# Kernel tuning notes

Measured on AMD Instinct MI355X. Metric: run time of the kernel, lower is better.

The kernel has to match this reference:

```python
import jax, jax.numpy as jnp
import numpy as np

WS = (8, 8)          # window_size
HEADS = 8
DH = 64              # dim_head
SHIFT = (4, 4)
SCALE = DH ** -0.5


def setup_inputs() -> dict:
    key = jax.random.key(0)
    ks = jax.random.split(key, 5)
    dim = 64
    inner = HEADS * DH  # 512
    b, h, w = 4, 192, 192
    x = jax.random.normal(ks[0], (b, h, w, dim), dtype=jnp.float32)
    Wq = jax.random.normal(ks[1], (dim, inner), dtype=jnp.float32) * (dim ** -0.5)
    Wkv = jax.random.normal(ks[2], (dim, 2 * inner), dtype=jnp.float32) * (dim ** -0.5)
    Wo = jax.random.normal(ks[3], (inner, dim), dtype=jnp.float32) * (inner ** -0.5)
    bo = jnp.zeros((dim,), dtype=jnp.float32)
    seq_l = WS[0] * WS[1]
    pos_emb = jax.random.normal(ks[4], (1, HEADS, seq_l, seq_l), dtype=jnp.float32)
    return {"x": x, "Wq": Wq, "Wkv": Wkv, "Wo": Wo, "bo": bo, "pos_emb": pos_emb}


def reference(x, Wq, Wkv, Wo, bo, pos_emb):
    b, h, w, c = x.shape
    L = WS[0] * WS[1]  # 64 tokens per window
    if SHIFT[0] > 0:
        x = jnp.roll(x, shift=(-SHIFT[0], -SHIFT[1]), axis=(1, 2))
    # NOTE: original uses a raw .view() here (row-major reshape), NOT an 8x8
    # window partition. Replicate exactly.
    nw = b * (h // WS[0]) * (w // WS[1])
    x_inp = x.reshape(nw, L, c)                      # [nw, 64, c]
    q = x_inp @ Wq                                   # [nw, 64, inner]
    kv = x_inp @ Wkv
    k, v = jnp.split(kv, 2, axis=-1)
    # original: raw view (nw, L, inner) -> (nw, heads, L, dh) (not a transpose)
    q = q.reshape(nw, HEADS, L, DH) * SCALE
    k = k.reshape(nw, HEADS, L, DH)
    v = v.reshape(nw, HEADS, L, DH)
    sim = jnp.einsum('bhid,bhjd->bhij', q, k) + pos_emb
    attn = jax.nn.softmax(sim, axis=-1)
    out = jnp.einsum('bhij,bhjd->bhid', attn, v)     # [nw, heads, 64, dh]
    # original: raw view back to (nw, L, inner)
    out = out.reshape(nw, L, HEADS * DH)
    out = out @ Wo + bo                              # [nw, 64, c]
    out = out.reshape(b, h, w, c)
    if SHIFT[0] > 0:
        out = jnp.roll(out, shift=(SHIFT[0], SHIFT[1]), axis=(1, 2))
    return out
```

## Files before the change

kernel.cpp:

```cpp
#include <hip/hip_runtime.h>
#include <hip/hip_bf16.h>
#include <stdint.h>

typedef __attribute__((ext_vector_type(8))) short bf16x8;
typedef __attribute__((ext_vector_type(4))) short s16x4;
typedef __attribute__((ext_vector_type(4))) float f32x4;

#define THREADS 256
constexpr int NWIN = 2304;

constexpr int WCATT_E = 0;
constexpr int WOT_E   = 98304;
constexpr int POS_E   = 131072;
constexpr size_t WS_NEED = 327680;

__device__ __forceinline__ short f2bf(float f) {
  __hip_bfloat16 h = __float2bfloat16(f);
  return __builtin_bit_cast(short, h);
}
__device__ __forceinline__ float bf2f(short s) {
  uint32_t u = ((uint32_t)(uint16_t)s) << 16;
  return __builtin_bit_cast(float, u);
}
__device__ __forceinline__ int swz(int row, int h) {
  return ((((row ^ (row >> 2) ^ (row >> 3)) & 7) ^ h) << 4);
}

__global__ void wmsa_prep(const float* __restrict__ Wq, const float* __restrict__ Wkv,
                          const float* __restrict__ Wo, const float* __restrict__ pos,
                          short* __restrict__ ws) {
  int idx = blockIdx.x * 256 + threadIdx.x;
  if (idx < 32768) {
    int n = idx & 511, k = idx >> 9;
    ws[WCATT_E + n * 64 + k] = f2bf(Wq[k * 512 + n] * 0.125f);
  } else if (idx < 98304) {
    int j = idx - 32768;
    int nkv = j & 1023, k = j >> 10;
    ws[WCATT_E + (512 + nkv) * 64 + k] = f2bf(Wkv[k * 1024 + nkv]);
  } else if (idx < 131072) {
    int j = idx - 98304;
    int n = j & 63, k = j >> 6;
    ws[WOT_E + n * 512 + k] = f2bf(Wo[k * 64 + n]);
  } else if (idx < 163840) {
    int j = idx - 131072;
    ws[POS_E + j] = f2bf(pos[j]);
  }
}

__global__ __launch_bounds__(512, 2)
void wmsa_mfma4(const float* __restrict__ x, const float* __restrict__ bo,
                const short* __restrict__ ws, float* __restrict__ out) {
  extern __shared__ __align__(16) char lds[];
  const int tid = threadIdx.x;
  const int wv = tid >> 6;
  const int l  = tid & 63;
  const int lr = l & 15;
  const int lg = l >> 4;

  const int bid = blockIdx.x;
  const int q   = bid >> 2;
  const int hp  = bid & 3;

  bf16x8 xa[4][2];
  #pragma unroll
  for (int win = 0; win < 4; ++win) {
    int w   = 4 * q + win;
    int bb  = w / 576;
    int rem = (w % 576) * 64;
    int hh  = rem / 192;
    int ww0 = rem % 192;
    int src_h = (hh + 4) % 192;
    const float* xp = x + (size_t)(bb * 192 + src_h) * 12288;
    int tok = 16 * hp + lr;
    int sw = ww0 + tok + 4; if (sw >= 192) sw -= 192;
    const float* xq = xp + sw * 64;
    #pragma unroll
    for (int ks = 0; ks < 2; ++ks) {
      float4 a = *(const float4*)(xq + ks * 32 + lg * 8);
      float4 b = *(const float4*)(xq + ks * 32 + lg * 8 + 4);
      bf16x8 v;
      v[0] = f2bf(a.x); v[1] = f2bf(a.y); v[2] = f2bf(a.z); v[3] = f2bf(a.w);
      v[4] = f2bf(b.x); v[5] = f2bf(b.y); v[6] = f2bf(b.z); v[7] = f2bf(b.w);
      xa[win][ks] = v;
    }
  }

  #pragma unroll
  for (int t = 0; t < 8; ++t) {
    int nt = wv + 8 * t;
    int nload = nt * 16 + lr;
    bf16x8 b0 = *(const bf16x8*)(ws + WCATT_E + nload * 64 + lg * 8);
    bf16x8 b1 = *(const bf16x8*)(ws + WCATT_E + nload * 64 + 32 + lg * 8);
    const bool isQ = (t < 4);
    int i  = (lr & 7) * 8 + ((nt >> 2) & 7);
    int h2 = lr >> 3;
    int d0 = (nt & 3) * 16 + lg * 4;
    int off = (isQ ? 0 : 16384) + h2 * 8192 + i * 128 + ((d0 * 2) ^ swz(i, h2));
    #pragma unroll
    for (int win = 0; win < 4; ++win) {
      f32x4 acc = {0.f, 0.f, 0.f, 0.f};
      acc = __builtin_amdgcn_mfma_f32_16x16x32_bf16(b0, xa[win][0], acc, 0, 0, 0);
      acc = __builtin_amdgcn_mfma_f32_16x16x32_bf16(b1, xa[win][1], acc, 0, 0, 0);
      s16x4 pk;
      #pragma unroll
      for (int r = 0; r < 4; ++r) pk[r] = f2bf(acc[r]);
      *(s16x4*)(lds + win * 32768 + off) = pk;
    }
  }

  const int bq = wv & 3, aq = wv >> 2;
  f32x4 vacc[4][4];
  #pragma unroll
  for (int u = 0; u < 4; ++u) {
    int ntile = (aq * 4 + u) * 4 + bq;
    int nload = (64 + ntile) * 16 + lr;
    bf16x8 b0 = *(const bf16x8*)(ws + WCATT_E + nload * 64 + lg * 8);
    bf16x8 b1 = *(const bf16x8*)(ws + WCATT_E + nload * 64 + 32 + lg * 8);
    #pragma unroll
    for (int win = 0; win < 4; ++win) {
      f32x4 acc = {0.f, 0.f, 0.f, 0.f};
      acc = __builtin_amdgcn_mfma_f32_16x16x32_bf16(xa[win][0], b0, acc, 0, 0, 0);
      acc = __builtin_amdgcn_mfma_f32_16x16x32_bf16(xa[win][1], b1, acc, 0, 0, 0);
      vacc[win][u] = acc;
    }
  }
  __syncthreads();

  const int hl = (wv >> 1) & 1;
  const int ih = wv & 1;
  const int hglob = 2 * hp + hl;
  const int wbase = aq;

  s16x4 posr[2][4];
  #pragma unroll
  for (int it = 0; it < 2; ++it) {
    int i = (ih * 2 + it) * 16 + lr;
    const short* pp = ws + POS_E + hglob * 4096 + i * 64;
    #pragma unroll
    for (int jt = 0; jt < 4; ++jt)
      posr[it][jt] = *(const s16x4*)(pp + jt * 16 + lg * 4);
  }

  #pragma unroll
  for (int c = 0; c < 2; ++c) {
    char* ldw = lds + (wbase + 2 * c) * 32768;
    f32x4 s[2][4];
    #pragma unroll
    for (int it = 0; it < 2; ++it)
      #pragma unroll
      for (int jt = 0; jt < 4; ++jt) s[it][jt] = (f32x4){0.f, 0.f, 0.f, 0.f};

    #pragma unroll
    for (int ks = 0; ks < 2; ++ks) {
      bf16x8 kb[4], qa[2];
      #pragma unroll
      for (int jt = 0; jt < 4; ++jt) {
        int j = jt * 16 + lr;
        kb[jt] = *(const bf16x8*)(ldw + 16384 + hl * 8192 + j * 128 + ((ks * 64 + lg * 16) ^ swz(j, hl)));
      }
      #pragma unroll
      for (int it = 0; it < 2; ++it) {
        int i = (ih * 2 + it) * 16 + lr;
        qa[it] = *(const bf16x8*)(ldw + hl * 8192 + i * 128 + ((ks * 64 + lg * 16) ^ swz(i, hl)));
      }
      __builtin_amdgcn_s_setprio(1);
      #pragma unroll
      for (int it = 0; it < 2; ++it)
        #pragma unroll
        for (int jt = 0; jt < 4; ++jt)
          s[it][jt] = __builtin_amdgcn_mfma_f32_16x16x32_bf16(kb[jt], qa[it], s[it][jt], 0, 0, 0);
      __builtin_amdgcn_s_setprio(0);
    }

    #pragma unroll
    for (int it = 0; it < 2; ++it) {
      int i = (ih * 2 + it) * 16 + lr;
      float sum = 0.f;
      #pragma unroll
      for (int jt = 0; jt < 4; ++jt)
        #pragma unroll
        for (int r = 0; r < 4; ++r) {
          float pv = __expf(s[it][jt][r] + bf2f(posr[it][jt][r]));
          s[it][jt][r] = pv;
          sum += pv;
        }
      sum += __shfl_xor(sum, 16);
      sum += __shfl_xor(sum, 32);
      float rinv = 1.f / sum;
      #pragma unroll
      for (int jt = 0; jt < 4; ++jt) {
        s16x4 pk;
        #pragma unroll
        for (int r = 0; r < 4; ++r) pk[r] = f2bf(s[it][jt][r] * rinv);
        *(s16x4*)(ldw + hl * 8192 + i * 128 + ((jt * 32 + lg * 8) ^ swz(i, hl))) = pk;
      }
    }
  }
  __syncthreads();

  {
    int d = bq * 16 + lr;
    #pragma unroll
    for (int win = 0; win < 4; ++win)
      #pragma unroll
      for (int r = 0; r < 4; ++r) {
        int tl = lg * 4 + r;
        int h2 = tl >> 3;
        int jb = (tl & 7) * 16 + aq * 8;
        s16x4 pk;
        #pragma unroll
        for (int u = 0; u < 4; ++u) pk[u] = f2bf(vacc[win][u][r]);
        *(s16x4*)(lds + win * 32768 + 16384 + h2 * 8192 + d * 128 + (jb ^ swz(d, h2))) = pk;
      }
  }
  __syncthreads();

  bf16x8 wofr[16];
  #pragma unroll
  for (int ks = 0; ks < 16; ++ks)
    wofr[ks] = *(const bf16x8*)(ws + WOT_E + (bq * 16 + lr) * 512 + ks * 32 + lg * 8);

  #pragma unroll
  for (int c = 0; c < 2; ++c) {
    char* ldw = lds + (wbase + 2 * c) * 32768;
    f32x4 o[2][4];
    #pragma unroll
    for (int it = 0; it < 2; ++it)
      #pragma unroll
      for (int dt = 0; dt < 4; ++dt) o[it][dt] = (f32x4){0.f, 0.f, 0.f, 0.f};
    #pragma unroll
    for (int ks = 0; ks < 2; ++ks) {
      bf16x8 vb[4], pa[2];
      #pragma unroll
      for (int dt = 0; dt < 4; ++dt) {
        int d = dt * 16 + lr;
        vb[dt] = *(const bf16x8*)(ldw + 16384 + hl * 8192 + d * 128 + ((ks * 64 + lg * 16) ^ swz(d, hl)));
      }
      #pragma unroll
      for (int it = 0; it < 2; ++it) {
        int i = (ih * 2 + it) * 16 + lr;
        pa[it] = *(const bf16x8*)(ldw + hl * 8192 + i * 128 + ((ks * 64 + lg * 16) ^ swz(i, hl)));
      }
      __builtin_amdgcn_s_setprio(1);
      #pragma unroll
      for (int it = 0; it < 2; ++it)
        #pragma unroll
        for (int dt = 0; dt < 4; ++dt)
          o[it][dt] = __builtin_amdgcn_mfma_f32_16x16x32_bf16(vb[dt], pa[it], o[it][dt], 0, 0, 0);
      __builtin_amdgcn_s_setprio(0);
    }
    #pragma unroll
    for (int it = 0; it < 2; ++it) {
      int i  = (ih * 2 + it) * 16 + lr;
      int lm = 8 * hl + (i >> 3);
      int rp = lm * 8 + (i & 7);
      #pragma unroll
      for (int dt = 0; dt < 4; ++dt) {
        s16x4 pk;
        #pragma unroll
        for (int r = 0; r < 4; ++r) pk[r] = f2bf(o[it][dt][r]);
        *(s16x4*)(ldw + rp * 128 + ((dt * 32 + lg * 8) ^ swz(rp, 0))) = pk;
      }
    }
  }
  __syncthreads();

  f32x4 oacc0 = {0.f, 0.f, 0.f, 0.f};
  f32x4 oacc1 = {0.f, 0.f, 0.f, 0.f};
  #pragma unroll
  for (int ks = 0; ks < 16; ++ks) {
    int rp = lr * 8 + (ks >> 1);
    int boff = rp * 128 + (((ks & 1) * 64 + lg * 16) ^ swz(rp, 0));
    bf16x8 bA = *(const bf16x8*)(lds + wbase * 32768 + boff);
    bf16x8 bB = *(const bf16x8*)(lds + (wbase + 2) * 32768 + boff);
    oacc0 = __builtin_amdgcn_mfma_f32_16x16x32_bf16(wofr[ks], bA, oacc0, 0, 0, 0);
    oacc1 = __builtin_amdgcn_mfma_f32_16x16x32_bf16(wofr[ks], bB, oacc1, 0, 0, 0);
  }
  {
    int c0 = bq * 16 + lg * 4;
    float4 bo4 = *(const float4*)(bo + c0);
    int tok = 16 * hp + lr;
    #pragma unroll
    for (int c = 0; c < 2; ++c) {
      int w   = 4 * q + wbase + 2 * c;
      int bb  = w / 576;
      int rem = (w % 576) * 64;
      int hh  = rem / 192;
      int ww0 = rem % 192;
      int src_h = (hh + 4) % 192;
      float* orow = out + (size_t)(bb * 192 + src_h) * 12288;
      int sw = ww0 + tok + 4; if (sw >= 192) sw -= 192;
      f32x4 oa = c ? oacc1 : oacc0;
      float4 ov;
      ov.x = oa[0] + bo4.x; ov.y = oa[1] + bo4.y;
      ov.z = oa[2] + bo4.z; ov.w = oa[3] + bo4.w;
      *(float4*)(orow + sw * 64 + c0) = ov;
    }
  }
}

__global__ __launch_bounds__(THREADS, 2)
void wmsa_mfma(const float* __restrict__ x, const float* __restrict__ bo,
               const short* __restrict__ ws, float* __restrict__ out) {
  __shared__ __align__(16) char lds[65536];
  const int tid = threadIdx.x;
  const int wv = tid >> 6;
  const int l  = tid & 63;
  const int lr = l & 15;
  const int lg = l >> 4;

  const int bid = blockIdx.x;
  const int p   = bid >> 2;
  const int hp  = bid & 3;

  const float* xrow[2];
  float* orow[2];
  int ww0a[2];
  #pragma unroll
  for (int win = 0; win < 2; ++win) {
    int w   = 2 * p + win;
    int t0  = w * 64;
    int bb  = t0 / 36864;
    int rem = t0 % 36864;
    int hh  = rem / 192;
    ww0a[win] = rem % 192;
    int src_h = (hh + 4) % 192;
    xrow[win] = x + (size_t)(bb * 192 + src_h) * 12288;
    orow[win] = out + (size_t)(bb * 192 + src_h) * 12288;
  }

  bf16x8 xa[2][2];
  #pragma unroll
  for (int win = 0; win < 2; ++win) {
    int tok = 16 * hp + lr;
    int sw = ww0a[win] + tok + 4; if (sw >= 192) sw -= 192;
    const float* xp = xrow[win] + sw * 64;
    #pragma unroll
    for (int ks = 0; ks < 2; ++ks) {
      float4 a = *(const float4*)(xp + ks * 32 + lg * 8);
      float4 b = *(const float4*)(xp + ks * 32 + lg * 8 + 4);
      bf16x8 v;
      v[0] = f2bf(a.x); v[1] = f2bf(a.y); v[2] = f2bf(a.z); v[3] = f2bf(a.w);
      v[4] = f2bf(b.x); v[5] = f2bf(b.y); v[6] = f2bf(b.z); v[7] = f2bf(b.w);
      xa[win][ks] = v;
    }
  }

  #pragma unroll 4
  for (int t = 0; t < 16; ++t) {
    int nt = wv + 4 * t;
    int nload = nt * 16 + lr;
    bf16x8 b0 = *(const bf16x8*)(ws + WCATT_E + nload * 64 + lg * 8);
    bf16x8 b1 = *(const bf16x8*)(ws + WCATT_E + nload * 64 + 32 + lg * 8);
    const bool isQ = (t < 8);
    int i  = (lr & 7) * 8 + (t & 7);
    int h2 = lr >> 3;
    int d0 = wv * 16 + lg * 4;
    int off = (isQ ? 0 : 16384) + h2 * 8192 + i * 128 + ((d0 * 2) ^ swz(i, h2));
    #pragma unroll
    for (int win = 0; win < 2; ++win) {
      f32x4 acc = {0.f, 0.f, 0.f, 0.f};
      acc = __builtin_amdgcn_mfma_f32_16x16x32_bf16(b0, xa[win][0], acc, 0, 0, 0);
      acc = __builtin_amdgcn_mfma_f32_16x16x32_bf16(b1, xa[win][1], acc, 0, 0, 0);
      s16x4 pk;
      #pragma unroll
      for (int r = 0; r < 4; ++r) pk[r] = f2bf(acc[r]);
      *(s16x4*)(lds + win * 32768 + off) = pk;
    }
  }

  f32x4 vacc[2][8];
  #pragma unroll
  for (int tv = 0; tv < 8; ++tv) {
    int nload = (64 + wv + 4 * tv) * 16 + lr;
    bf16x8 b0 = *(const bf16x8*)(ws + WCATT_E + nload * 64 + lg * 8);
    bf16x8 b1 = *(const bf16x8*)(ws + WCATT_E + nload * 64 + 32 + lg * 8);
    #pragma unroll
    for (int win = 0; win < 2; ++win) {
      f32x4 acc = {0.f, 0.f, 0.f, 0.f};
      acc = __builtin_amdgcn_mfma_f32_16x16x32_bf16(xa[win][0], b0, acc, 0, 0, 0);
      acc = __builtin_amdgcn_mfma_f32_16x16x32_bf16(xa[win][1], b1, acc, 0, 0, 0);
      vacc[win][tv] = acc;
    }
  }
  __syncthreads();

  const int hl = wv >> 1;
  const int ih = wv & 1;
  const int hglob = 2 * hp + hl;

  s16x4 posr[2][4];
  #pragma unroll
  for (int it = 0; it < 2; ++it) {
    int i = (ih * 2 + it) * 16 + lr;
    const short* pp = ws + POS_E + hglob * 4096 + i * 64;
    #pragma unroll
    for (int jt = 0; jt < 4; ++jt)
      posr[it][jt] = *(const s16x4*)(pp + jt * 16 + lg * 4);
  }

  #pragma unroll
  for (int win = 0; win < 2; ++win) {
    char* ldw = lds + win * 32768;
    f32x4 s[2][4];
    #pragma unroll
    for (int it = 0; it < 2; ++it)
      #pragma unroll
      for (int jt = 0; jt < 4; ++jt) s[it][jt] = (f32x4){0.f, 0.f, 0.f, 0.f};

    #pragma unroll
    for (int ks = 0; ks < 2; ++ks) {
      bf16x8 kb[4], qa[2];
      #pragma unroll
      for (int jt = 0; jt < 4; ++jt) {
        int j = jt * 16 + lr;
        kb[jt] = *(const bf16x8*)(ldw + 16384 + hl * 8192 + j * 128 + ((ks * 64 + lg * 16) ^ swz(j, hl)));
      }
      #pragma unroll
      for (int it = 0; it < 2; ++it) {
        int i = (ih * 2 + it) * 16 + lr;
        qa[it] = *(const bf16x8*)(ldw + hl * 8192 + i * 128 + ((ks * 64 + lg * 16) ^ swz(i, hl)));
      }
      __builtin_amdgcn_s_setprio(1);
      #pragma unroll
      for (int it = 0; it < 2; ++it)
        #pragma unroll
        for (int jt = 0; jt < 4; ++jt)
          s[it][jt] = __builtin_amdgcn_mfma_f32_16x16x32_bf16(kb[jt], qa[it], s[it][jt], 0, 0, 0);
      __builtin_amdgcn_s_setprio(0);
    }

    #pragma unroll
    for (int it = 0; it < 2; ++it) {
      int i = (ih * 2 + it) * 16 + lr;
      float sum = 0.f;
      #pragma unroll
      for (int jt = 0; jt < 4; ++jt)
        #pragma unroll
        for (int r = 0; r < 4; ++r) {
          float pv = __expf(s[it][jt][r] + bf2f(posr[it][jt][r]));
          s[it][jt][r] = pv;
          sum += pv;
        }
      sum += __shfl_xor(sum, 16);
      sum += __shfl_xor(sum, 32);
      float rinv = 1.f / sum;
      #pragma unroll
      for (int jt = 0; jt < 4; ++jt) {
        s16x4 pk;
        #pragma unroll
        for (int r = 0; r < 4; ++r) pk[r] = f2bf(s[it][jt][r] * rinv);
        *(s16x4*)(ldw + hl * 8192 + i * 128 + ((jt * 32 + lg * 8) ^ swz(i, hl))) = pk;
      }
    }
  }
  __syncthreads();

  {
    int d = wv * 16 + lr;
    #pragma unroll
    for (int win = 0; win < 2; ++win)
      #pragma unroll
      for (int r = 0; r < 4; ++r) {
        int tl = lg * 4 + r;
        int h2 = tl >> 3;
        int slot = tl & 7;
        bf16x8 pk;
        #pragma unroll
        for (int tv = 0; tv < 8; ++tv) pk[tv] = f2bf(vacc[win][tv][r]);
        *(bf16x8*)(lds + win * 32768 + 16384 + h2 * 8192 + d * 128 + ((slot * 16) ^ swz(d, h2))) = pk;
      }
  }
  __syncthreads();

  bf16x8 wofr[16];
  #pragma unroll
  for (int ks = 0; ks < 16; ++ks)
    wofr[ks] = *(const bf16x8*)(ws + WOT_E + (wv * 16 + lr) * 512 + ks * 32 + lg * 8);

  #pragma unroll
  for (int win = 0; win < 2; ++win) {
    char* ldw = lds + win * 32768;
    f32x4 o[2][4];
    #pragma unroll
    for (int it = 0; it < 2; ++it)
      #pragma unroll
      for (int dt = 0; dt < 4; ++dt) o[it][dt] = (f32x4){0.f, 0.f, 0.f, 0.f};
    #pragma unroll
    for (int ks = 0; ks < 2; ++ks) {
      bf16x8 vb[4], pa[2];
      #pragma unroll
      for (int dt = 0; dt < 4; ++dt) {
        int d = dt * 16 + lr;
        vb[dt] = *(const bf16x8*)(ldw + 16384 + hl * 8192 + d * 128 + ((ks * 64 + lg * 16) ^ swz(d, hl)));
      }
      #pragma unroll
      for (int it = 0; it < 2; ++it) {
        int i = (ih * 2 + it) * 16 + lr;
        pa[it] = *(const bf16x8*)(ldw + hl * 8192 + i * 128 + ((ks * 64 + lg * 16) ^ swz(i, hl)));
      }
      __builtin_amdgcn_s_setprio(1);
      #pragma unroll
      for (int it = 0; it < 2; ++it)
        #pragma unroll
        for (int dt = 0; dt < 4; ++dt)
          o[it][dt] = __builtin_amdgcn_mfma_f32_16x16x32_bf16(vb[dt], pa[it], o[it][dt], 0, 0, 0);
      __builtin_amdgcn_s_setprio(0);
    }
    #pragma unroll
    for (int it = 0; it < 2; ++it) {
      int i  = (ih * 2 + it) * 16 + lr;
      int lm = 8 * hl + (i >> 3);
      int rp = lm * 8 + (i & 7);
      #pragma unroll
      for (int dt = 0; dt < 4; ++dt) {
        s16x4 pk;
        #pragma unroll
        for (int r = 0; r < 4; ++r) pk[r] = f2bf(o[it][dt][r]);
        *(s16x4*)(ldw + rp * 128 + ((dt * 32 + lg * 8) ^ swz(rp, 0))) = pk;
      }
    }
  }
  __syncthreads();

  f32x4 oacc[2];
  oacc[0] = (f32x4){0.f, 0.f, 0.f, 0.f};
  oacc[1] = (f32x4){0.f, 0.f, 0.f, 0.f};
  #pragma unroll
  for (int ks = 0; ks < 16; ++ks) {
    int rp = lr * 8 + (ks >> 1);
    int boff = rp * 128 + (((ks & 1) * 64 + lg * 16) ^ swz(rp, 0));
    #pragma unroll
    for (int win = 0; win < 2; ++win) {
      bf16x8 bfrOH = *(const bf16x8*)(lds + win * 32768 + boff);
      oacc[win] = __builtin_amdgcn_mfma_f32_16x16x32_bf16(wofr[ks], bfrOH, oacc[win], 0, 0, 0);
    }
  }
  {
    int c0 = wv * 16 + lg * 4;
    float4 bo4 = *(const float4*)(bo + c0);
    int tok = 16 * hp + lr;
    #pragma unroll
    for (int win = 0; win < 2; ++win) {
      int sw = ww0a[win] + tok + 4; if (sw >= 192) sw -= 192;
      float4 ov;
      ov.x = oacc[win][0] + bo4.x; ov.y = oacc[win][1] + bo4.y;
      ov.z = oacc[win][2] + bo4.z; ov.w = oacc[win][3] + bo4.w;
      *(float4*)(orow[win] + sw * 64 + c0) = ov;
    }
  }
}

extern "C" void kernel_launch(void* const* d_in, const int* in_sizes, int n_in,
                              void* d_out, int out_size, void* d_ws, size_t ws_size,
                              hipStream_t stream) {
  const float* x    = (const float*)d_in[0];
  const float* Wq   = (const float*)d_in[1];
  const float* Wkv  = (const float*)d_in[2];
  const float* Wo   = (const float*)d_in[3];
  const float* bo   = (const float*)d_in[4];
  const float* pos  = (const float*)d_in[5];
  float* o = (float*)d_out;
  wmsa_prep<<<dim3(640), dim3(256), 0, stream>>>(Wq, Wkv, Wo, pos, (short*)d_ws);
  hipError_t e = hipFuncSetAttribute((const void*)wmsa_mfma4,
                                     hipFuncAttributeMaxDynamicSharedMemorySize, 131072);
  if (e == hipSuccess) {
    wmsa_mfma4<<<dim3(NWIN), dim3(512), 131072, stream>>>(x, bo, (const short*)d_ws, o);
  } else {
    wmsa_mfma<<<dim3(NWIN * 2), dim3(THREADS), 0, stream>>>(x, bo, (const short*)d_ws, o);
  }
}
```

Baseline: 175.6 us.

## Software-pipeline window pairs so projection of one pair overlaps attention of other

Splits the four windows per block into two pairs and staggers their stages: the QKV projection for the second pair is interleaved with the attention, softmax and PV of the first pair, and output projection of pair A is issued before PV of pair B. The goal is to fill MFMA and LDS idle time between barriers with independent work from the other pair. In exchange, weight fragments (qkw, vw) and accumulators stay live in registers longer, which raises register pressure and may cause spills at the 512-thread launch bound.

New measurement: 228.4 us. +30.1%, slower.

```diff
diff --git a/kernel.cpp b/kernel.cpp
--- a/kernel.cpp
+++ b/kernel.cpp
@@ -48,8 +48,8 @@
 }
 
 __global__ __launch_bounds__(512, 2)
-void wmsa_mfma4(const float* __restrict__ x, const float* __restrict__ bo,
-                const short* __restrict__ ws, float* __restrict__ out) {
+void wmsa_pipe(const float* __restrict__ x, const float* __restrict__ bo,
+               const short* __restrict__ ws, float* __restrict__ out) {
   extern __shared__ __align__(16) char lds[];
   const int tid = threadIdx.x;
   const int wv = tid >> 6;
@@ -60,6 +60,12 @@
   const int bid = blockIdx.x;
   const int q   = bid >> 2;
   const int hp  = bid & 3;
+
+  const int bq = wv & 3, aq = wv >> 2;
+  const int aw = aq;
+  const int hl = (wv >> 1) & 1;
+  const int ih = wv & 1;
+  const int hglob = 2 * hp + hl;
 
   bf16x8 xa[4][2];
   #pragma unroll
@@ -85,6 +91,16 @@
     }
   }
 
+  s16x4 posr[2][4];
+  #pragma unroll
+  for (int it = 0; it < 2; ++it) {
+    int i = (ih * 2 + it) * 16 + lr;
+    const short* pp = ws + POS_E + hglob * 4096 + i * 64;
+    #pragma unroll
+    for (int jt = 0; jt < 4; ++jt)
+      posr[it][jt] = *(const s16x4*)(pp + jt * 16 + lg * 4);
+  }
+
   #pragma unroll
   for (int t = 0; t < 8; ++t) {
     int nt = wv + 8 * t;
@@ -97,7 +113,7 @@
     int d0 = (nt & 3) * 16 + lg * 4;
     int off = (isQ ? 0 : 16384) + h2 * 8192 + i * 128 + ((d0 * 2) ^ swz(i, h2));
     #pragma unroll
-    for (int win = 0; win < 4; ++win) {
+    for (int win = 0; win < 2; ++win) {
       f32x4 acc = {0.f, 0.f, 0.f, 0.f};
       acc = __builtin_amdgcn_mfma_f32_16x16x32_bf16(b0, xa[win][0], acc, 0, 0, 0);
       acc = __builtin_amdgcn_mfma_f32_16x16x32_bf16(b1, xa[win][1], acc, 0, 0, 0);
@@ -107,9 +123,7 @@
       *(s16x4*)(lds + win * 32768 + off) = pk;
     }
   }
-
-  const int bq = wv & 3, aq = wv >> 2;
-  f32x4 vacc[4][4];
+  f32x4 vaccA[2][4];
   #pragma unroll
   for (int u = 0; u < 4; ++u) {
     int ntile = (aq * 4 + u) * 4 + bq;
@@ -117,91 +131,119 @@
     bf16x8 b0 = *(const bf16x8*)(ws + WCATT_E + nload * 64 + lg * 8);
     bf16x8 b1 = *(const bf16x8*)(ws + WCATT_E + nload * 64 + 32 + lg * 8);
     #pragma unroll
-    for (int win = 0; win < 4; ++win) {
+    for (int win = 0; win < 2; ++win) {
       f32x4 acc = {0.f, 0.f, 0.f, 0.f};
       acc = __builtin_amdgcn_mfma_f32_16x16x32_bf16(xa[win][0], b0, acc, 0, 0, 0);
       acc = __builtin_amdgcn_mfma_f32_16x16x32_bf16(xa[win][1], b1, acc, 0, 0, 0);
-      vacc[win][u] = acc;
-    }
-  }
-  __syncthreads();
-
-  const int hl = (wv >> 1) & 1;
-  const int ih = wv & 1;
-  const int hglob = 2 * hp + hl;
-  const int wbase = aq;
-
-  s16x4 posr[2][4];
+      vaccA[win][u] = acc;
+    }
+  }
+  __syncthreads();
+
+  char* ldwA = lds + aw * 32768;
+
+  bf16x8 qkw[8][2];
+  #pragma unroll
+  for (int t = 0; t < 8; ++t) {
+    int nload = (wv + 8 * t) * 16 + lr;
+    qkw[t][0] = *(const bf16x8*)(ws + WCATT_E + nload * 64 + lg * 8);
+    qkw[t][1] = *(const bf16x8*)(ws + WCATT_E + nload * 64 + 32 + lg * 8);
+  }
+
+  f32x4 sA[2][4];
+  #pragma unroll
+  for (int it = 0; it < 2; ++it)
+    #pragma unroll
+    for (int jt = 0; jt < 4; ++jt) sA[it][jt] = (f32x4){0.f, 0.f, 0.f, 0.f};
+  #pragma unroll
+  for (int ks = 0; ks < 2; ++ks) {
+    bf16x8 kb[4], qa[2];
+    #pragma unroll
+    for (int jt = 0; jt < 4; ++jt) {
+      int j = jt * 16 + lr;
+      kb[jt] = *(const bf16x8*)(ldwA + 16384 + hl * 8192 + j * 128 + ((ks * 64 + lg * 16) ^ swz(j, hl)));
+    }
+    #pragma unroll
+    for (int it = 0; it < 2; ++it) {
+      int i = (ih * 2 + it) * 16 + lr;
+      qa[it] = *(const bf16x8*)(ldwA + hl * 8192 + i * 128 + ((ks * 64 + lg * 16) ^ swz(i, hl)));
+    }
+    __builtin_amdgcn_s_setprio(1);
+    #pragma unroll
+    for (int it = 0; it < 2; ++it)
+      #pragma unroll
+      for (int jt = 0; jt < 4; ++jt)
+        sA[it][jt] = __builtin_amdgcn_mfma_f32_16x16x32_bf16(kb[jt], qa[it], sA[it][jt], 0, 0, 0);
+    __builtin_amdgcn_s_setprio(0);
+  }
+
+  #pragma unroll
+  for (int t = 0; t < 8; ++t) {
+    int nt = wv + 8 * t;
+    const bool isQ = (t < 4);
+    int i  = (lr & 7) * 8 + ((nt >> 2) & 7);
+    int h2 = lr >> 3;
+    int d0 = (nt & 3) * 16 + lg * 4;
+    int off = (isQ ? 0 : 16384) + h2 * 8192 + i * 128 + ((d0 * 2) ^ swz(i, h2));
+    #pragma unroll
+    for (int win = 2; win < 4; ++win) {
+      f32x4 acc = {0.f, 0.f, 0.f, 0.f};
+      acc = __builtin_amdgcn_mfma_f32_16x16x32_bf16(qkw[t][0], xa[win][0], acc, 0, 0, 0);
+      acc = __builtin_amdgcn_mfma_f32_16x16x32_bf16(qkw[t][1], xa[win][1], acc, 0, 0, 0);
+      s16x4 pk;
+      #pragma unroll
+      for (int r = 0; r < 4; ++r) pk[r] = f2bf(acc[r]);
+      *(s16x4*)(lds + win * 32768 + off) = pk;
+    }
+  }
+
+  bf16x8 vw[4][2];
+  #pragma unroll
+  for (int u = 0; u < 4; ++u) {
+    int ntile = (aq * 4 + u) * 4 + bq;
+    int nload = (64 + ntile) * 16 + lr;
+    vw[u][0] = *(const bf16x8*)(ws + WCATT_E + nload * 64 + lg * 8);
+    vw[u][1] = *(const bf16x8*)(ws + WCATT_E + nload * 64 + 32 + lg * 8);
+  }
   #pragma unroll
   for (int it = 0; it < 2; ++it) {
     int i = (ih * 2 + it) * 16 + lr;
-    const short* pp = ws + POS_E + hglob * 4096 + i * 64;
+    float sum = 0.f;
     #pragma unroll
     for (int jt = 0; jt < 4; ++jt)
-      posr[it][jt] = *(const s16x4*)(pp + jt * 16 + lg * 4);
-  }
-
-  #pragma unroll
-  for (int c = 0; c < 2; ++c) {
-    char* ldw = lds + (wbase + 2 * c) * 32768;
-    f32x4 s[2][4];
-    #pragma unroll
-    for (int it = 0; it < 2; ++it)
-      #pragma unroll
-      for (int jt = 0; jt < 4; ++jt) s[it][jt] = (f32x4){0.f, 0.f, 0.f, 0.f};
-
-    #pragma unroll
-    for (int ks = 0; ks < 2; ++ks) {
-      bf16x8 kb[4], qa[2];
-      #pragma unroll
-      for (int jt = 0; jt < 4; ++jt) {
-        int j = jt * 16 + lr;
-        kb[jt] = *(const bf16x8*)(ldw + 16384 + hl * 8192 + j * 128 + ((ks * 64 + lg * 16) ^ swz(j, hl)));
-      }
-      #pragma unroll
-      for (int it = 0; it < 2; ++it) {
-        int i = (ih * 2 + it) * 16 + lr;
-        qa[it] = *(const bf16x8*)(ldw + hl * 8192 + i * 128 + ((ks * 64 + lg * 16) ^ swz(i, hl)));
-      }
-      __builtin_amdgcn_s_setprio(1);
-      #pragma unroll
-      for (int it = 0; it < 2; ++it)
-        #pragma unroll
-        for (int jt = 0; jt < 4; ++jt)
-          s[it][jt] = __builtin_amdgcn_mfma_f32_16x16x32_bf16(kb[jt], qa[it], s[it][jt], 0, 0, 0);
-      __builtin_amdgcn_s_setprio(0);
-    }
-
-    #pragma unroll
-    for (int it = 0; it < 2; ++it) {
-      int i = (ih * 2 + it) * 16 + lr;
-      float sum = 0.f;
-      #pragma unroll
-      for (int jt = 0; jt < 4; ++jt)
-        #pragma unroll
-        for (int r = 0; r < 4; ++r) {
-          float pv = __expf(s[it][jt][r] + bf2f(posr[it][jt][r]));
-          s[it][jt][r] = pv;
-          sum += pv;
-        }
-      sum += __shfl_xor(sum, 16);
-      sum += __shfl_xor(sum, 32);
-      float rinv = 1.f / sum;
-      #pragma unroll
-      for (int jt = 0; jt < 4; ++jt) {
-        s16x4 pk;
-        #pragma unroll
-        for (int r = 0; r < 4; ++r) pk[r] = f2bf(s[it][jt][r] * rinv);
-        *(s16x4*)(ldw + hl * 8192 + i * 128 + ((jt * 32 + lg * 8) ^ swz(i, hl))) = pk;
-      }
-    }
-  }
+      #pragma unroll
+      for (int r = 0; r < 4; ++r) {
+        float pv = __expf(sA[it][jt][r] + bf2f(posr[it][jt][r]));
+        sA[it][jt][r] = pv;
+        sum += pv;
+      }
+    sum += __shfl_xor(sum, 16);
+    sum += __shfl_xor(sum, 32);
+    float rinv = 1.f / sum;
+    #pragma unroll
+    for (int jt = 0; jt < 4; ++jt) {
+      s16x4 pk;
+      #pragma unroll
+      for (int r = 0; r < 4; ++r) pk[r] = f2bf(sA[it][jt][r] * rinv);
+      *(s16x4*)(ldwA + hl * 8192 + i * 128 + ((jt * 32 + lg * 8) ^ swz(i, hl))) = pk;
+    }
+  }
+  f32x4 vaccB[2][4];
+  #pragma unroll
+  for (int u = 0; u < 4; ++u)
+    #pragma unroll
+    for (int win = 2; win < 4; ++win) {
+      f32x4 acc = {0.f, 0.f, 0.f, 0.f};
+      acc = __builtin_amdgcn_mfma_f32_16x16x32_bf16(xa[win][0], vw[u][0], acc, 0, 0, 0);
+      acc = __builtin_amdgcn_mfma_f32_16x16x32_bf16(xa[win][1], vw[u][1], acc, 0, 0, 0);
+      vaccB[win - 2][u] = acc;
+    }
   __syncthreads();
 
   {
     int d = bq * 16 + lr;
     #pragma unroll
-    for (int win = 0; win < 4; ++win)
+    for (int win = 0; win < 2; ++win)
       #pragma unroll
       for (int r = 0; r < 4; ++r) {
         int tl = lg * 4 + r;
@@ -209,9 +251,59 @@
         int jb = (tl & 7) * 16 + aq * 8;
         s16x4 pk;
         #pragma unroll
-        for (int u = 0; u < 4; ++u) pk[u] = f2bf(vacc[win][u][r]);
+        for (int u = 0; u < 4; ++u) pk[u] = f2bf(vaccA[win][u][r]);
         *(s16x4*)(lds + win * 32768 + 16384 + h2 * 8192 + d * 128 + (jb ^ swz(d, h2))) = pk;
       }
+  }
+  char* ldwB = lds + (aw + 2) * 32768;
+  f32x4 sB[2][4];
+  #pragma unroll
+  for (int it = 0; it < 2; ++it)
+    #pragma unroll
+    for (int jt = 0; jt < 4; ++jt) sB[it][jt] = (f32x4){0.f, 0.f, 0.f, 0.f};
+  #pragma unroll
+  for (int ks = 0; ks < 2; ++ks) {
+    bf16x8 kb[4], qa[2];
+    #pragma unroll
+    for (int jt = 0; jt < 4; ++jt) {
+      int j = jt * 16 + lr;
+      kb[jt] = *(const bf16x8*)(ldwB + 16384 + hl * 8192 + j * 128 + ((ks * 64 + lg * 16) ^ swz(j, hl)));
+    }
+    #pragma unroll
+    for (int it = 0; it < 2; ++it) {
+      int i = (ih * 2 + it) * 16 + lr;
+      qa[it] = *(const bf16x8*)(ldwB + hl * 8192 + i * 128 + ((ks * 64 + lg * 16) ^ swz(i, hl)));
+    }
+    __builtin_amdgcn_s_setprio(1);
+    #pragma unroll
+    for (int it = 0; it < 2; ++it)
+      #pragma unroll
+      for (int jt = 0; jt < 4; ++jt)
+        sB[it][jt] = __builtin_amdgcn_mfma_f32_16x16x32_bf16(kb[jt], qa[it], sB[it][jt], 0, 0, 0);
+    __builtin_amdgcn_s_setprio(0);
+  }
+  #pragma unroll
+  for (int it = 0; it < 2; ++it) {
+    int i = (ih * 2 + it) * 16 + lr;
+    float sum = 0.f;
+    #pragma unroll
+    for (int jt = 0; jt < 4; ++jt)
+      #pragma unroll
+      for (int r = 0; r < 4; ++r) {
+        float pv = __expf(sB[it][jt][r] + bf2f(posr[it][jt][r]));
+        sB[it][jt][r] = pv;
+        sum += pv;
+      }
+    sum += __shfl_xor(sum, 16);
+    sum += __shfl_xor(sum, 32);
+    float rinv = 1.f / sum;
+    #pragma unroll
+    for (int jt = 0; jt < 4; ++jt) {
+      s16x4 pk;
+      #pragma unroll
+      for (int r = 0; r < 4; ++r) pk[r] = f2bf(sB[it][jt][r] * rinv);
+      *(s16x4*)(ldwB + hl * 8192 + i * 128 + ((jt * 32 + lg * 8) ^ swz(i, hl))) = pk;
+    }
   }
   __syncthreads();
 
@@ -220,9 +312,7 @@
   for (int ks = 0; ks < 16; ++ks)
     wofr[ks] = *(const bf16x8*)(ws + WOT_E + (bq * 16 + lr) * 512 + ks * 32 + lg * 8);
 
-  #pragma unroll
-  for (int c = 0; c < 2; ++c) {
-    char* ldw = lds + (wbase + 2 * c) * 32768;
+  {
     f32x4 o[2][4];
     #pragma unroll
     for (int it = 0; it < 2; ++it)
@@ -234,12 +324,12 @@
       #pragma unroll
       for (int dt = 0; dt < 4; ++dt) {
         int d = dt * 16 + lr;
-        vb[dt] = *(const bf16x8*)(ldw + 16384 + hl * 8192 + d * 128 + ((ks * 64 + lg * 16) ^ swz(d, hl)));
+        vb[dt] = *(const bf16x8*)(ldwA + 16384 + hl * 8192 + d * 128 + ((ks * 64 + lg * 16) ^ swz(d, hl)));
       }
       #pragma unroll
       for (int it = 0; it < 2; ++it) {
         int i = (ih * 2 + it) * 16 + lr;
-        pa[it] = *(const bf16x8*)(ldw + hl * 8192 + i * 128 + ((ks * 64 + lg * 16) ^ swz(i, hl)));
+        pa[it] = *(const bf16x8*)(ldwA + hl * 8192 + i * 128 + ((ks * 64 + lg * 16) ^ swz(i, hl)));
       }
       __builtin_amdgcn_s_setprio(1);
       #pragma unroll
@@ -259,43 +349,119 @@
         s16x4 pk;
         #pragma unroll
         for (int r = 0; r < 4; ++r) pk[r] = f2bf(o[it][dt][r]);
-        *(s16x4*)(ldw + rp * 128 + ((dt * 32 + lg * 8) ^ swz(rp, 0))) = pk;
-      }
-    }
-  }
-  __syncthreads();
-
-  f32x4 oacc0 = {0.f, 0.f, 0.f, 0.f};
-  f32x4 oacc1 = {0.f, 0.f, 0.f, 0.f};
-  #pragma unroll
-  for (int ks = 0; ks < 16; ++ks) {
-    int rp = lr * 8 + (ks >> 1);
-    int boff = rp * 128 + (((ks & 1) * 64 + lg * 16) ^ swz(rp, 0));
-    bf16x8 bA = *(const bf16x8*)(lds + wbase * 32768 + boff);
-    bf16x8 bB = *(const bf16x8*)(lds + (wbase + 2) * 32768 + boff);
-    oacc0 = __builtin_amdgcn_mfma_f32_16x16x32_bf16(wofr[ks], bA, oacc0, 0, 0, 0);
-    oacc1 = __builtin_amdgcn_mfma_f32_16x16x32_bf16(wofr[ks], bB, oacc1, 0, 0, 0);
+        *(s16x4*)(ldwA + rp * 128 + ((dt * 32 + lg * 8) ^ swz(rp, 0))) = pk;
+      }
+    }
   }
   {
+    int d = bq * 16 + lr;
+    #pragma unroll
+    for (int win = 2; win < 4; ++win)
+      #pragma unroll
+      for (int r = 0; r < 4; ++r) {
+        int tl = lg * 4 + r;
+        int h2 = tl >> 3;
+        int jb = (tl & 7) * 16 + aq * 8;
+        s16x4 pk;
+        #pragma unroll
+        for (int u = 0; u < 4; ++u) pk[u] = f2bf(vaccB[win - 2][u][r]);
+        *(s16x4*)(lds + win * 32768 + 16384 + h2 * 8192 + d * 128 + (jb ^ swz(d, h2))) = pk;
+      }
+  }
+  __syncthreads();
+
+  {
+    f32x4 oacc = {0.f, 0.f, 0.f, 0.f};
+    #pragma unroll
+    for (int ks = 0; ks < 16; ++ks) {
+      int rp = lr * 8 + (ks >> 1);
+      int boff = rp * 128 + (((ks & 1) * 64 + lg * 16) ^ swz(rp, 0));
+      bf16x8 bA = *(const bf16x8*)(lds + aw * 32768 + boff);
+      oacc = __builtin_amdgcn_mfma_f32_16x16x32_bf16(wofr[ks], bA, oacc, 0, 0, 0);
+    }
     int c0 = bq * 16 + lg * 4;
     float4 bo4 = *(const float4*)(bo + c0);
+    int w   = 4 * q + aw;
+    int bb  = w / 576;
+    int rem = (w % 576) * 64;
+    int hh  = rem / 192;
+    int ww0 = rem % 192;
+    int src_h = (hh + 4) % 192;
+    float* orow = out + (size_t)(bb * 192 + src_h) * 12288;
     int tok = 16 * hp + lr;
-    #pragma unroll
-    for (int c = 0; c < 2; ++c) {
-      int w   = 4 * q + wbase + 2 * c;
-      int bb  = w / 576;
-      int rem = (w % 576) * 64;
-      int hh  = rem / 192;
-      int ww0 = rem % 192;
-      int src_h = (hh + 4) % 192;
-      float* orow = out + (size_t)(bb * 192 + src_h) * 12288;
-      int sw = ww0 + tok + 4; if (sw >= 192) sw -= 192;
-      f32x4 oa = c ? oacc1 : oacc0;
-      float4 ov;
-      ov.x = oa[0] + bo4.x; ov.y = oa[1] + bo4.y;
-      ov.z = oa[2] + bo4.z; ov.w = oa[3] + bo4.w;
-      *(float4*)(orow + sw * 64 + c0) = ov;
-    }
+    int sw = ww0 + tok + 4; if (sw >= 192) sw -= 192;
+    float4 ov;
+    ov.x = oacc[0] + bo4.x; ov.y = oacc[1] + bo4.y;
+    ov.z = oacc[2] + bo4.z; ov.w = oacc[3] + bo4.w;
+    *(float4*)(orow + sw * 64 + c0) = ov;
+  }
+  {
+    f32x4 o[2][4];
+    #pragma unroll
+    for (int it = 0; it < 2; ++it)
+      #pragma unroll
+      for (int dt = 0; dt < 4; ++dt) o[it][dt] = (f32x4){0.f, 0.f, 0.f, 0.f};
+    #pragma unroll
+    for (int ks = 0; ks < 2; ++ks) {
+      bf16x8 vb[4], pa[2];
+      #pragma unroll
+      for (int dt = 0; dt < 4; ++dt) {
+        int d = dt * 16 + lr;
+        vb[dt] = *(const bf16x8*)(ldwB + 16384 + hl * 8192 + d * 128 + ((ks * 64 + lg * 16) ^ swz(d, hl)));
+      }
+      #pragma unroll
+      for (int it = 0; it < 2; ++it) {
+        int i = (ih * 2 + it) * 16 + lr;
+        pa[it] = *(const bf16x8*)(ldwB + hl * 8192 + i * 128 + ((ks * 64 + lg * 16) ^ swz(i, hl)));
+      }
+      __builtin_amdgcn_s_setprio(1);
+      #pragma unroll
+      for (int it = 0; it < 2; ++it)
+        #pragma unroll
+        for (int dt = 0; dt < 4; ++dt)
+          o[it][dt] = __builtin_amdgcn_mfma_f32_16x16x32_bf16(vb[dt], pa[it], o[it][dt], 0, 0, 0);
+      __builtin_amdgcn_s_setprio(0);
+    }
+    #pragma unroll
+    for (int it = 0; it < 2; ++it) {
+      int i  = (ih * 2 + it) * 16 + lr;
+      int lm = 8 * hl + (i >> 3);
+      int rp = lm * 8 + (i & 7);
+      #pragma unroll
+      for (int dt = 0; dt < 4; ++dt) {
+        s16x4 pk;
+        #pragma unroll
+        for (int r = 0; r < 4; ++r) pk[r] = f2bf(o[it][dt][r]);
+        *(s16x4*)(ldwB + rp * 128 + ((dt * 32 + lg * 8) ^ swz(rp, 0))) = pk;
+      }
+    }
+  }
+  __syncthreads();
+
+  {
+    f32x4 oacc = {0.f, 0.f, 0.f, 0.f};
+    #pragma unroll
+    for (int ks = 0; ks < 16; ++ks) {
+      int rp = lr * 8 + (ks >> 1);
+      int boff = rp * 128 + (((ks & 1) * 64 + lg * 16) ^ swz(rp, 0));
+      bf16x8 bB = *(const bf16x8*)(lds + (aw + 2) * 32768 + boff);
+      oacc = __builtin_amdgcn_mfma_f32_16x16x32_bf16(wofr[ks], bB, oacc, 0, 0, 0);
+    }
+    int c0 = bq * 16 + lg * 4;
+    float4 bo4 = *(const float4*)(bo + c0);
+    int w   = 4 * q + aw + 2;
+    int bb  = w / 576;
+    int rem = (w % 576) * 64;
+    int hh  = rem / 192;
+    int ww0 = rem % 192;
+    int src_h = (hh + 4) % 192;
+    float* orow = out + (size_t)(bb * 192 + src_h) * 12288;
+    int tok = 16 * hp + lr;
+    int sw = ww0 + tok + 4; if (sw >= 192) sw -= 192;
+    float4 ov;
+    ov.x = oacc[0] + bo4.x; ov.y = oacc[1] + bo4.y;
+    ov.z = oacc[2] + bo4.z; ov.w = oacc[3] + bo4.w;
+    *(float4*)(orow + sw * 64 + c0) = ov;
   }
 }
 
@@ -562,10 +728,10 @@
   const float* pos  = (const float*)d_in[5];
   float* o = (float*)d_out;
   wmsa_prep<<<dim3(640), dim3(256), 0, stream>>>(Wq, Wkv, Wo, pos, (short*)d_ws);
-  hipError_t e = hipFuncSetAttribute((const void*)wmsa_mfma4,
+  hipError_t e = hipFuncSetAttribute((const void*)wmsa_pipe,
                                      hipFuncAttributeMaxDynamicSharedMemorySize, 131072);
   if (e == hipSuccess) {
-    wmsa_mfma4<<<dim3(NWIN), dim3(512), 131072, stream>>>(x, bo, (const short*)d_ws, o);
+    wmsa_pipe<<<dim3(NWIN), dim3(512), 131072, stream>>>(x, bo, (const short*)d_ws, o);
   } else {
     wmsa_mfma<<<dim3(NWIN * 2), dim3(THREADS), 0, stream>>>(x, bo, (const short*)d_ws, o);
   }
```
